# Optimization experiments

Measured on AMD Instinct MI355X. Metric: run time of the kernel, lower is better.

The kernel has to match this reference:

```python
import jax, jax.numpy as jnp
import numpy as np

B, S, T = 64, 49, 32
ENC, HID, EMB, VOCAB = 512, 512, 512, 32000
ATT = HID  # attention_dim = hidden_size in __init__


def setup_inputs() -> dict:
    key = jax.random.key(0)
    ks = jax.random.split(key, 20)
    def lin(k, out_d, in_d):
        s = 1.0 / np.sqrt(in_d)
        kw, kb = jax.random.split(k)
        return (jax.random.uniform(kw, (out_d, in_d), jnp.float32, -s, s),
                jax.random.uniform(kb, (out_d,), jnp.float32, -s, s))
    W_ih, b_ih = lin(ks[0], 3 * HID, EMB + ENC)
    W_hh, b_hh = lin(ks[1], 3 * HID, HID)
    W_out, b_out = lin(ks[2], VOCAB, HID)
    W_init, b_init = lin(ks[3], HID, ENC)
    W_beta, b_beta = lin(ks[4], ENC, HID)
    W_ea, b_ea = lin(ks[5], ATT, ENC)
    W_da, b_da = lin(ks[6], ATT, HID)
    W_fa, b_fa = lin(ks[7], 1, ATT)
    emb = jax.random.normal(ks[8], (VOCAB, EMB), jnp.float32)
    feats = jax.random.normal(ks[9], (B, S, ENC), jnp.float32)
    seq = jax.random.randint(ks[10], (B, T), 0, VOCAB)
    length = jax.random.randint(ks[11], (B,), 1, T + 1).at[0].set(T)
    return dict(feats=feats, seq=seq, length=length, emb=emb,
                W_ih=W_ih, b_ih=b_ih, W_hh=W_hh, b_hh=b_hh,
                W_out=W_out, b_out=b_out, W_init=W_init, b_init=b_init,
                W_beta=W_beta, b_beta=b_beta, W_ea=W_ea, b_ea=b_ea,
                W_da=W_da, b_da=b_da, W_fa=W_fa, b_fa=b_fa)


def _forward(feats, seq, length, emb, W_ih, b_ih, W_hh, b_hh, W_out, b_out,
             W_init, b_init, W_beta, b_beta, W_ea, b_ea, W_da, b_da, W_fa, b_fa):
    Tlen = seq.shape[1]
    embed_seq = emb[seq]                      # [B, T, EMB]
    embed_seq = jnp.swapaxes(embed_seq, 0, 1)  # [T, B, EMB]
    # active[t, b] = (length[b] > t); equivalent to torch's sorted shrinking batch
    active = (jnp.arange(Tlen)[:, None] < length[None, :])  # [T, B] bool
    h0 = jnp.mean(feats, axis=1) @ W_init.T + b_init         # [B, HID]
    scope0 = jnp.ones(feats.shape[:2], feats.dtype)          # [B, S]
    att1 = feats @ W_ea.T + b_ea                              # [B, S, ATT], hoisted

    def gru_cell(x, h):
        gi = x @ W_ih.T + b_ih
        gh = h @ W_hh.T + b_hh
        ir, iz, inn = jnp.split(gi, 3, axis=1)
        hr, hz, hn = jnp.split(gh, 3, axis=1)
        r = jax.nn.sigmoid(ir + hr)
        z = jax.nn.sigmoid(iz + hz)
        n = jnp.tanh(inn + r * hn)
        return (1.0 - z) * n + z * h

    def step(carry, xs):
        h, scope = carry
        embed_t, act = xs                     # [B, EMB], [B] bool
        actf = act[:, None].astype(h.dtype)
        att2 = h @ W_da.T + b_da              # [B, ATT]
        att = (jax.nn.relu(att1 + att2[:, None, :]) @ W_fa.T).squeeze(-1) + b_fa  # [B, S]
        alpha = jax.nn.softmax(att, axis=1)
        alpha_tilde = scope * alpha
        scope = jnp.where(act[:, None], scope * (1.0 - alpha), scope)
        awe = jnp.einsum('bse,bs->be', feats, alpha)          # [B, ENC]
        gate = jax.nn.sigmoid(h @ W_beta.T + b_beta)
        x = jnp.concatenate([embed_t, gate * awe], axis=1)
        h_new = gru_cell(x, h)
        h = jnp.where(act[:, None], h_new, h)
        preds = h_new @ W_out.T + b_out
        out_t = preds * actf
        alpha_out = alpha_tilde * actf
        return (h, scope), (out_t, alpha_out)

    (_, _), (output, alphas) = jax.lax.scan(step, (h0, scope0), (embed_seq, active))
    output = jnp.swapaxes(output, 0, 1)   # [B, T, VOCAB]
    alphas = jnp.swapaxes(alphas, 0, 1)   # [B, T, S]
    return output, alphas


def reference(feats, seq, length, emb, W_ih, b_ih, W_hh, b_hh, W_out, b_out,
              W_init, b_init, W_beta, b_beta, W_ea, b_ea, W_da, b_da, W_fa, b_fa):
    return _forward(feats, seq, length, emb, W_ih, b_ih, W_hh, b_hh, W_out, b_out,
                    W_init, b_init, W_beta, b_beta, W_ea, b_ea, W_da, b_da, W_fa, b_fa)
```

## Files before the change

### kernel.cpp

```cpp
#include <hip/hip_runtime.h>
#include <cstdint>
#include <cstddef>

#define B_   64
#define S_   49
#define T_   32
#define D_   512
#define V_   32000
#define G3   1536
#define NBLK 64

typedef float v4f   __attribute__((ext_vector_type(4)));
typedef int   i32x4 __attribute__((ext_vector_type(4)));
typedef _Float16 f16;
typedef _Float16 f16x8 __attribute__((ext_vector_type(8)));
typedef _Float16 f16x4 __attribute__((ext_vector_type(4)));

__device__ __forceinline__ float sigm(float x) { return 1.f / (1.f + __expf(-x)); }

__device__ __forceinline__ uint64_t ld_a64(const void* p) {
  return __hip_atomic_load((const uint64_t*)p, __ATOMIC_RELAXED, __HIP_MEMORY_SCOPE_AGENT);
}
__device__ __forceinline__ void st_a64(void* p, uint64_t v) {
  __hip_atomic_store((uint64_t*)p, v, __ATOMIC_RELAXED, __HIP_MEMORY_SCOPE_AGENT);
}
__device__ __forceinline__ uint32_t ld_a32(const void* p) {
  return __hip_atomic_load((const uint32_t*)p, __ATOMIC_RELAXED, __HIP_MEMORY_SCOPE_AGENT);
}
__device__ __forceinline__ void st_a32(void* p, uint32_t v) {
  __hip_atomic_store((uint32_t*)p, v, __ATOMIC_RELAXED, __HIP_MEMORY_SCOPE_AGENT);
}

__global__ __launch_bounds__(256) void k_cvt16(const float* __restrict__ in,
                                               f16* __restrict__ out) {
  int i = (blockIdx.x * 256 + threadIdx.x) * 8;
  float4 a = *(const float4*)(in + i);
  float4 b = *(const float4*)(in + i + 4);
  f16x8 o;
  o[0] = (f16)a.x; o[1] = (f16)a.y; o[2] = (f16)a.z; o[3] = (f16)a.w;
  o[4] = (f16)b.x; o[5] = (f16)b.y; o[6] = (f16)b.z; o[7] = (f16)b.w;
  *(f16x8*)(out + i) = o;
}

__global__ __launch_bounds__(128) void k_embed(const float* __restrict__ emb,
    const int* __restrict__ seq, const int* __restrict__ length,
    f16* __restrict__ xemb16, float* __restrict__ actmask) {
  int m = blockIdx.x;
  int t = m >> 6, b = m & 63;
  int idx = seq[b * T_ + t];
  float4 v = ((const float4*)(emb + (size_t)idx * D_))[threadIdx.x];
  f16x4 o;
  o[0] = (f16)v.x; o[1] = (f16)v.y; o[2] = (f16)v.z; o[3] = (f16)v.w;
  *(f16x4*)(xemb16 + (size_t)m * D_ + threadIdx.x * 4) = o;
  if (threadIdx.x == 0) actmask[b * T_ + t] = (t < length[b]) ? 1.f : 0.f;
}

__global__ __launch_bounds__(256) void k_hmean(const float* __restrict__ feats,
    float* __restrict__ hmean) {
  int b = blockIdx.x, tid = threadIdx.x;
  for (int e = tid; e < D_; e += 256) {
    float s = 0.f;
    for (int si = 0; si < S_; ++si) s += feats[((size_t)b * S_ + si) * D_ + e];
    hmean[b * D_ + e] = s * (1.f / 49.f);
  }
}

__global__ __launch_bounds__(256) void k_gemm_f32(
    float* __restrict__ C, const float* __restrict__ X, const float* __restrict__ W,
    const float* __restrict__ bias, int N, int K, int ldw) {
  __shared__ __align__(16) float XsT[32][68];
  __shared__ __align__(16) float WsT[32][68];
  const int nbase = blockIdx.x * 64, mbase = blockIdx.y * 64;
  const int tid = threadIdx.x;
  const int lr = tid >> 2;
  const int lk = (tid & 3) * 8;
  const int ty = tid >> 4, tx = tid & 15;
  float acc[4][4] = {};
  for (int k0 = 0; k0 < K; k0 += 32) {
    {
      const float* xs = X + (size_t)(mbase + lr) * K + k0 + lk;
      const float* wsrc = W + (size_t)(nbase + lr) * ldw + k0 + lk;
      float4 x0 = *(const float4*)xs, x1 = *(const float4*)(xs + 4);
      float4 w0 = *(const float4*)wsrc, w1 = *(const float4*)(wsrc + 4);
      XsT[lk + 0][lr] = x0.x; XsT[lk + 1][lr] = x0.y; XsT[lk + 2][lr] = x0.z; XsT[lk + 3][lr] = x0.w;
      XsT[lk + 4][lr] = x1.x; XsT[lk + 5][lr] = x1.y; XsT[lk + 6][lr] = x1.z; XsT[lk + 7][lr] = x1.w;
      WsT[lk + 0][lr] = w0.x; WsT[lk + 1][lr] = w0.y; WsT[lk + 2][lr] = w0.z; WsT[lk + 3][lr] = w0.w;
      WsT[lk + 4][lr] = w1.x; WsT[lk + 5][lr] = w1.y; WsT[lk + 6][lr] = w1.z; WsT[lk + 7][lr] = w1.w;
    }
    __syncthreads();
    #pragma unroll
    for (int kk = 0; kk < 32; ++kk) {
      float4 a4 = *(const float4*)&XsT[kk][ty * 4];
      float4 w4 = *(const float4*)&WsT[kk][tx * 4];
      float av[4] = {a4.x, a4.y, a4.z, a4.w};
      float wv[4] = {w4.x, w4.y, w4.z, w4.w};
      #pragma unroll
      for (int i = 0; i < 4; ++i)
        #pragma unroll
        for (int j = 0; j < 4; ++j)
          acc[i][j] = fmaf(av[i], wv[j], acc[i][j]);
    }
    __syncthreads();
  }
  #pragma unroll
  for (int i = 0; i < 4; ++i) {
    int m = mbase + ty * 4 + i;
    int n = nbase + tx * 4;
    float4 o;
    o.x = acc[i][0] + bias[n + 0];
    o.y = acc[i][1] + bias[n + 1];
    o.z = acc[i][2] + bias[n + 2];
    o.w = acc[i][3] + bias[n + 3];
    *(float4*)&C[(size_t)m * N + n] = o;
  }
}

__global__ __launch_bounds__(256) void k_gemm16b(
    const f16* __restrict__ A, const f16* __restrict__ Bw,
    const float* __restrict__ bias, float* __restrict__ out, int N) {
  __shared__ __align__(16) f16 As[128 * 32];
  __shared__ __align__(16) f16 Bs[128 * 32];
  const int nb = blockIdx.x * 128, mb = blockIdx.y * 128;
  const int tid = threadIdx.x;
  const int l = tid & 63, w = tid >> 6;
  const int wr = w >> 1, wc = w & 1;
  const int lm = l & 15;
  const int kc = l >> 4;
  const int rchunk = (kc ^ ((lm >> 1) & 3)) * 8;
  v4f acc[4][4];
  #pragma unroll
  for (int mi = 0; mi < 4; ++mi)
    #pragma unroll
    for (int ni = 0; ni < 4; ++ni)
      acc[mi][ni] = (v4f){0.f, 0.f, 0.f, 0.f};
  i32x4 ra[2], rb[2];
  auto LD = [&](int k0) {
    #pragma unroll
    for (int i = 0; i < 2; ++i) {
      int ch = i * 256 + tid;
      int row = ch >> 2, cq = ch & 3;
      ra[i] = *(const i32x4*)&A[(size_t)(mb + row) * 512 + k0 + cq * 8];
      rb[i] = *(const i32x4*)&Bw[(size_t)(nb + row) * 512 + k0 + cq * 8];
    }
  };
  LD(0);
  for (int k0 = 0; k0 < 512; k0 += 32) {
    #pragma unroll
    for (int i = 0; i < 2; ++i) {
      int ch = i * 256 + tid;
      int row = ch >> 2, cq = ch & 3;
      int sc = (cq ^ ((row >> 1) & 3)) * 8;
      *(i32x4*)&As[row * 32 + sc] = ra[i];
      *(i32x4*)&Bs[row * 32 + sc] = rb[i];
    }
    __syncthreads();
    if (k0 < 480) LD(k0 + 32);
    f16x8 af[4], bf[4];
    #pragma unroll
    for (int mi = 0; mi < 4; ++mi)
      af[mi] = *(const f16x8*)&As[(wr * 64 + mi * 16 + lm) * 32 + rchunk];
    #pragma unroll
    for (int ni = 0; ni < 4; ++ni)
      bf[ni] = *(const f16x8*)&Bs[(wc * 64 + ni * 16 + lm) * 32 + rchunk];
    #pragma unroll
    for (int mi = 0; mi < 4; ++mi)
      #pragma unroll
      for (int ni = 0; ni < 4; ++ni)
        acc[mi][ni] = __builtin_amdgcn_mfma_f32_16x16x32_f16(af[mi], bf[ni], acc[mi][ni], 0, 0, 0);
    __syncthreads();
  }
  #pragma unroll
  for (int ni = 0; ni < 4; ++ni) {
    int n = nb + wc * 64 + ni * 16 + lm;
    float bo = bias[n];
    #pragma unroll
    for (int mi = 0; mi < 4; ++mi) {
      int m0 = mb + wr * 64 + mi * 16 + (l >> 4) * 4;
      #pragma unroll
      for (int r = 0; r < 4; ++r)
        out[(size_t)(m0 + r) * N + n] = acc[mi][ni][r] + bo;
    }
  }
}

__global__ __launch_bounds__(256) void k_packW(
    const float* __restrict__ Wda, const float* __restrict__ Wbe,
    const float* __restrict__ Whh, const float* __restrict__ Wih,
    f16* __restrict__ Wp1, f16* __restrict__ Wp2, f16* __restrict__ Wp3) {
  int K = blockIdx.x, tid = threadIdx.x;
  for (int idx = tid; idx < 40 * 512; idx += 256) {
    int r = idx >> 9, e = idx & 511;
    float v;
    if (r < 8)       v = Wda[(size_t)(8 * K + r) * D_ + e];
    else if (r < 16) v = Wbe[(size_t)(8 * K + r - 8) * D_ + e];
    else if (r < 24) v = Whh[(size_t)(8 * K + r - 16) * D_ + e];
    else if (r < 32) v = Whh[(size_t)(512 + 8 * K + r - 24) * D_ + e];
    else             v = Whh[(size_t)(1024 + 8 * K + r - 32) * D_ + e];
    Wp1[(size_t)K * 20480 + idx] = (f16)v;
  }
  for (int idx = tid; idx < 24 * 512; idx += 256) {
    int r = idx >> 9, e = idx & 511;
    int g = r >> 3, jj = r & 7;
    float v = Wih[(size_t)(g * 512 + 8 * K + jj) * 1024 + 512 + e];
    Wp2[(size_t)K * 12288 + idx] = (f16)v;
  }
  for (int idx = tid; idx < 24 * 512; idx += 256) {
    int rl = idx >> 9, e = idx & 511;
    int r = K * 24 + rl;
    Wp3[(size_t)r * 512 + e] = (f16)Wih[(size_t)r * 1024 + e];
  }
}

__global__ __launch_bounds__(256) void k_packF(
    const float* __restrict__ feats, const float* __restrict__ att1,
    const float* __restrict__ h0,
    f16* __restrict__ feats16, f16* __restrict__ att116, f16* __restrict__ h16) {
  const int NF = B_ * S_ * D_;
  for (size_t i = blockIdx.x * 256 + threadIdx.x; i < 2 * NF + B_ * D_;
       i += (size_t)gridDim.x * 256) {
    if (i < NF)           feats16[i] = (f16)feats[i];
    else if (i < 2 * NF)  att116[i - NF] = (f16)att1[i - NF];
    else                  h16[i - 2 * NF] = (f16)h0[i - 2 * NF];
  }
}

__global__ __launch_bounds__(256) void k_packG(
    const float* __restrict__ gi_embed, float* __restrict__ gi_pack) {
  for (size_t i = blockIdx.x * 256 + threadIdx.x; i < (size_t)T_ * 64 * 32 * 64;
       i += (size_t)gridDim.x * 256) {
    int b = i & 63;
    int slot = (i >> 6) & 31;
    int Kb = (i >> 11) & 63;
    int t = i >> 17;
    if (slot < 24) {
      int g8 = slot >> 3, jj = slot & 7;
      gi_pack[i] = gi_embed[((size_t)t * 64 + b) * G3 + g8 * 512 + 8 * Kb + jj];
    }
  }
}

__device__ __forceinline__ void wait_flags64(const int* __restrict__ flags,
                                             int target, int tid) {
  if (tid < 64) {
    while (!__all((int)ld_a32(flags + tid * 16) >= target))
      __builtin_amdgcn_s_sleep(2);
  }
  __syncthreads();
}

__device__ __forceinline__ void set_flag(int* slot, int val, int tid) {
  __syncthreads();
  if (tid == 0) st_a32(slot, (uint32_t)val);
}

__device__ __forceinline__ void stage_fast(const f16* __restrict__ src,
                                           uint4* __restrict__ hs, int tid) {
  const i32x4* s = (const i32x4*)src;
  #pragma unroll
  for (int half = 0; half < 2; ++half) {
    i32x4 v[8];
    #pragma unroll
    for (int i = 0; i < 8; ++i) {
      int g = (half * 8 + i) * 256 + tid;
      asm volatile("global_load_dwordx4 %0, %1, off sc0 sc1"
                   : "=v"(v[i]) : "v"(s + g));
    }
    asm volatile("s_waitcnt vmcnt(0)" ::: "memory");
    __builtin_amdgcn_sched_barrier(0);
    #pragma unroll
    for (int i = 0; i < 8; ++i) {
      int g = (half * 8 + i) * 256 + tid;
      int b = g >> 6, c = g & 63;
      *(i32x4*)&hs[b * 64 + (c ^ (b & 7))] = v[i];
    }
  }
}

__global__ __launch_bounds__(256, 1) void k_recur(
    const f16* __restrict__ Wp1, const f16* __restrict__ Wp2,
    const f16* __restrict__ att116, const f16* __restrict__ feats16,
    const float* __restrict__ gi_pack,
    const float* __restrict__ b_da, const float* __restrict__ b_beta,
    const float* __restrict__ b_hh,
    const float* __restrict__ W_fa, const float* __restrict__ b_fa,
    const int* __restrict__ length,
    f16* __restrict__ h16, f16* __restrict__ xg16,
    float* __restrict__ att2g,
    float* __restrict__ alphas, f16* __restrict__ Hbuf,
    int* __restrict__ flags) {
  __shared__ __align__(16) uint4 lds_all[8704];
  __shared__ float gh_lds[24 * 72];
  __shared__ float gix_lds[24 * 72];
  __shared__ float att2_s[512];
  __shared__ float gate_s[512];
  __shared__ float att_s[64];
  __shared__ float alpha_s[64];
  uint4* hs = lds_all;
  uint4* W1 = lds_all + 4096;
  uint4* W2 = lds_all + 6656;
  float* attp = (float*)(lds_all + 8192);

  const int K = blockIdx.x, tid = threadIdx.x;
  const int w = tid >> 6, l = tid & 63;
  const int lm = l & 15, c4 = l >> 4;
  const int bq = tid & 63, jg = tid >> 6;
  const int jj0 = 2 * jg, jj1 = 2 * jg + 1;
  int* flagA = flags;
  int* flagB = flags + 1024;
  int* flagC = flags + 2048;

  {
    const uint4* s1 = (const uint4*)(Wp1 + (size_t)K * 20480);
    const uint4* s2 = (const uint4*)(Wp2 + (size_t)K * 12288);
    #pragma unroll
    for (int i = 0; i < 10; ++i) {
      int g = i * 256 + tid;
      int s = g >> 6, c = g & 63;
      W1[s * 64 + (c ^ (s & 7))] = s1[g];
    }
    #pragma unroll
    for (int i = 0; i < 6; ++i) {
      int g = i * 256 + tid;
      int s = g >> 6, c = g & 63;
      W2[s * 64 + (c ^ (s & 7))] = s2[g];
    }
  }
  const int lenB = length[K];
  const float bfa0 = b_fa[0];
  const int lb = length[bq];
  const float bhr0 = b_hh[8 * K + jj0],        bhr1 = b_hh[8 * K + jj1];
  const float bhz0 = b_hh[512 + 8 * K + jj0],  bhz1 = b_hh[512 + 8 * K + jj1];
  const float bhn0 = b_hh[1024 + 8 * K + jj0], bhn1 = b_hh[1024 + 8 * K + jj1];
  float scope_r = 1.f;
  __syncthreads();

  for (int t = 0; t < T_; ++t) {
    if (t) wait_flags64(flagC, t, tid);
    stage_fast(h16, hs, tid);
    __syncthreads();
    float hold0, hold1;
    {
      f16x8 hv = __builtin_bit_cast(f16x8, hs[bq * 64 + (K ^ (bq & 7))]);
      hold0 = (float)hv[jj0]; hold1 = (float)hv[jj1];
    }
    {
      v4f a0 = {0.f, 0.f, 0.f, 0.f};
      int bb = w * 16 + lm;
      #pragma unroll
      for (int kt = 0; kt < 16; ++kt) {
        int ca = kt * 4 + c4;
        f16x8 av = __builtin_bit_cast(f16x8, hs[bb * 64 + (ca ^ (bb & 7))]);
        f16x8 b0 = __builtin_bit_cast(f16x8, W1[lm * 64 + (ca ^ (lm & 7))]);
        a0 = __builtin_amdgcn_mfma_f32_16x16x32_f16(av, b0, a0, 0, 0, 0);
      }
      #pragma unroll
      for (int r = 0; r < 4; ++r)
        attp[(w * 16 + c4 * 4 + r) * 16 + lm] = a0[r];
    }
    __syncthreads();
    #pragma unroll
    for (int q = 0; q < 2; ++q) {
      int pp = tid * 2 + q;
      int bat = pp >> 3, pi = pp & 7;
      float2 f2;
      f2.x = attp[bat * 16 + 2 * pi];
      f2.y = attp[bat * 16 + 2 * pi + 1];
      size_t idx = (size_t)bat * 512 +
                   ((pi < 4) ? (4 * K + pi) : (256 + 4 * K + (pi - 4)));
      st_a64((uint64_t*)att2g + idx, __builtin_bit_cast(uint64_t, f2));
    }
    set_flag(flagA + K * 16, t + 1, tid);
    {
      v4f a1 = {0.f,0.f,0.f,0.f}, a2 = {0.f,0.f,0.f,0.f};
      int bb = w * 16 + lm;
      #pragma unroll
      for (int kt = 0; kt < 16; ++kt) {
        int ca = kt * 4 + c4;
        f16x8 av = __builtin_bit_cast(f16x8, hs[bb * 64 + (ca ^ (bb & 7))]);
        f16x8 b1 = __builtin_bit_cast(f16x8, W1[(16 + lm) * 64 + (ca ^ ((16 + lm) & 7))]);
        f16x8 b2 = __builtin_bit_cast(f16x8, W1[(32 + lm) * 64 + (ca ^ ((32 + lm) & 7))]);
        a1 = __builtin_amdgcn_mfma_f32_16x16x32_f16(av, b1, a1, 0, 0, 0);
        a2 = __builtin_amdgcn_mfma_f32_16x16x32_f16(av, b2, a2, 0, 0, 0);
      }
      #pragma unroll
      for (int r = 0; r < 4; ++r) {
        int bat = w * 16 + c4 * 4 + r;
        gh_lds[lm * 72 + bat] = a1[r];
        if (lm < 8) gh_lds[(16 + lm) * 72 + bat] = a2[r];
      }
    }
    wait_flags64(flagA, t + 1, tid);
    {
      bool act = t < lenB;
      const uint64_t* arow2 = (const uint64_t*)att2g + (size_t)K * 512;
      for (int c = tid; c < 512; c += 256) {
        float2 f = __builtin_bit_cast(float2, ld_a64(arow2 + c));
        int a0i = 2 * c;
        if (a0i < 512) {
          att2_s[a0i]     = f.x + b_da[a0i];
          att2_s[a0i + 1] = f.y + b_da[a0i + 1];
        } else {
          int gi = a0i - 512;
          gate_s[gi]     = sigm(f.x + b_beta[gi]);
          gate_s[gi + 1] = sigm(f.y + b_beta[gi + 1]);
        }
      }
      __syncthreads();
      for (int s = w; s < S_; s += 4) {
        const f16x8* arow = (const f16x8*)(att116 + ((size_t)K * S_ + s) * D_);
        int a0i = l * 8;
        f16x8 av = arow[l];
        float p = 0.f;
        #pragma unroll
        for (int jx = 0; jx < 8; ++jx) {
          float v = (float)av[jx] + att2_s[a0i + jx];
          v = v > 0.f ? v : 0.f;
          p = fmaf(v, W_fa[a0i + jx], p);
        }
        #pragma unroll
        for (int off = 32; off > 0; off >>= 1) p += __shfl_xor(p, off, 64);
        if (l == 0) att_s[s] = p + bfa0;
      }
      __syncthreads();
      if (tid < 64) {
        float x = (tid < S_) ? att_s[tid] : -1e30f;
        float m = x;
        #pragma unroll
        for (int off = 32; off > 0; off >>= 1) m = fmaxf(m, __shfl_xor(m, off, 64));
        float e = (tid < S_) ? __expf(x - m) : 0.f;
        float su = e;
        #pragma unroll
        for (int off = 32; off > 0; off >>= 1) su += __shfl_xor(su, off, 64);
        if (tid < S_) alpha_s[tid] = e / su;
      }
      __syncthreads();
      if (tid < S_) {
        float al = alpha_s[tid];
        alphas[((size_t)K * T_ + t) * S_ + tid] = act ? scope_r * al : 0.f;
        scope_r = act ? scope_r * (1.f - al) : scope_r;
      }
      if (tid < 128) {
        int e0 = tid * 4;
        float s0 = 0.f, s1 = 0.f, s2 = 0.f, s3 = 0.f;
        #pragma unroll 7
        for (int s = 0; s < S_; ++s) {
          float al = alpha_s[s];
          f16x4 fv = *(const f16x4*)(feats16 + ((size_t)K * S_ + s) * D_ + e0);
          s0 = fmaf(al, (float)fv[0], s0);
          s1 = fmaf(al, (float)fv[1], s1);
          s2 = fmaf(al, (float)fv[2], s2);
          s3 = fmaf(al, (float)fv[3], s3);
        }
        f16x4 o;
        o[0] = (f16)(gate_s[e0 + 0] * s0);
        o[1] = (f16)(gate_s[e0 + 1] * s1);
        o[2] = (f16)(gate_s[e0 + 2] * s2);
        o[3] = (f16)(gate_s[e0 + 3] * s3);
        st_a64((uint64_t*)xg16 + (size_t)K * 128 + tid,
               __builtin_bit_cast(uint64_t, o));
      }
    }
    set_flag(flagB + K * 16, t + 1, tid);
    wait_flags64(flagB, t + 1, tid);
    stage_fast(xg16, hs, tid);
    __syncthreads();
    {
      v4f c0 = {0.f,0.f,0.f,0.f}, c1 = {0.f,0.f,0.f,0.f};
      int bb = w * 16 + lm;
      #pragma unroll
      for (int kt = 0; kt < 16; ++kt) {
        int ca = kt * 4 + c4;
        f16x8 av = __builtin_bit_cast(f16x8, hs[bb * 64 + (ca ^ (bb & 7))]);
        f16x8 b0 = __builtin_bit_cast(f16x8, W2[lm * 64 + (ca ^ (lm & 7))]);
        f16x8 b1 = __builtin_bit_cast(f16x8, W2[(16 + lm) * 64 + (ca ^ ((16 + lm) & 7))]);
        c0 = __builtin_amdgcn_mfma_f32_16x16x32_f16(av, b0, c0, 0, 0, 0);
        c1 = __builtin_amdgcn_mfma_f32_16x16x32_f16(av, b1, c1, 0, 0, 0);
      }
      #pragma unroll
      for (int r = 0; r < 4; ++r) {
        int bat = w * 16 + c4 * 4 + r;
        gix_lds[lm * 72 + bat] = c0[r];
        if (lm < 8) gix_lds[(16 + lm) * 72 + bat] = c1[r];
      }
    }
    __syncthreads();
    {
      const float* gp = gi_pack + (size_t)(t * 64 + K) * 2048;
      float r0 = sigm(gix_lds[jj0 * 72 + bq] + gp[jj0 * 64 + bq] + gh_lds[jj0 * 72 + bq] + bhr0);
      float r1 = sigm(gix_lds[jj1 * 72 + bq] + gp[jj1 * 64 + bq] + gh_lds[jj1 * 72 + bq] + bhr1);
      float z0 = sigm(gix_lds[(8 + jj0) * 72 + bq] + gp[(8 + jj0) * 64 + bq] + gh_lds[(8 + jj0) * 72 + bq] + bhz0);
      float z1 = sigm(gix_lds[(8 + jj1) * 72 + bq] + gp[(8 + jj1) * 64 + bq] + gh_lds[(8 + jj1) * 72 + bq] + bhz1);
      float n0 = tanhf(gix_lds[(16 + jj0) * 72 + bq] + gp[(16 + jj0) * 64 + bq] + r0 * (gh_lds[(16 + jj0) * 72 + bq] + bhn0));
      float n1 = tanhf(gix_lds[(16 + jj1) * 72 + bq] + gp[(16 + jj1) * 64 + bq] + r1 * (gh_lds[(16 + jj1) * 72 + bq] + bhn1));
      float hn0 = (1.f - z0) * n0 + z0 * hold0;
      float hn1 = (1.f - z1) * n1 + z1 * hold1;
      bool act = t < lb;
      unsigned short u0 = __builtin_bit_cast(unsigned short, (f16)(act ? hn0 : hold0));
      unsigned short u1 = __builtin_bit_cast(unsigned short, (f16)(act ? hn1 : hold1));
      st_a32((uint32_t*)h16 + bq * 256 + 4 * K + jg,
             (uint32_t)u0 | ((uint32_t)u1 << 16));
      unsigned short p0 = __builtin_bit_cast(unsigned short, (f16)hn0);
      unsigned short p1 = __builtin_bit_cast(unsigned short, (f16)hn1);
      ((uint32_t*)Hbuf)[((size_t)bq * T_ + t) * 256 + 4 * K + jg] =
          (uint32_t)p0 | ((uint32_t)p1 << 16);
    }
    set_flag(flagC + K * 16, t + 1, tid);
  }
}

__global__ __launch_bounds__(256) void k_outgemm(
    const f16* __restrict__ Hb, const f16* __restrict__ Wb,
    const float* __restrict__ b_out, const float* __restrict__ actmask,
    float* __restrict__ out) {
  __shared__ __align__(16) f16 As[128 * 32];
  __shared__ __align__(16) f16 Bs[128 * 32];
  const int bid = blockIdx.x;
  const int swz = (bid & 7) * 500 + (bid >> 3);
  const int mb = (swz & 15) * 128;
  const int nb = (swz >> 4) * 128;
  const int tid = threadIdx.x;
  const int l = tid & 63, w = tid >> 6;
  const int wr = w >> 1, wc = w & 1;
  const int lm = l & 15;
  const int kc = l >> 4;
  const int rchunk = (kc ^ ((lm >> 1) & 3)) * 8;
  v4f acc[4][4];
  #pragma unroll
  for (int mi = 0; mi < 4; ++mi)
    #pragma unroll
    for (int ni = 0; ni < 4; ++ni)
      acc[mi][ni] = (v4f){0.f, 0.f, 0.f, 0.f};
  i32x4 ra[2], rb[2];
  auto LD = [&](int k0) {
    #pragma unroll
    for (int i = 0; i < 2; ++i) {
      int ch = i * 256 + tid;
      int row = ch >> 2, cq = ch & 3;
      ra[i] = *(const i32x4*)&Hb[(size_t)(mb + row) * 512 + k0 + cq * 8];
      rb[i] = *(const i32x4*)&Wb[(size_t)(nb + row) * 512 + k0 + cq * 8];
    }
  };
  LD(0);
  for (int k0 = 0; k0 < 512; k0 += 32) {
    #pragma unroll
    for (int i = 0; i < 2; ++i) {
      int ch = i * 256 + tid;
      int row = ch >> 2, cq = ch & 3;
      int sc = (cq ^ ((row >> 1) & 3)) * 8;
      *(i32x4*)&As[row * 32 + sc] = ra[i];
      *(i32x4*)&Bs[row * 32 + sc] = rb[i];
    }
    __syncthreads();
    if (k0 < 480) LD(k0 + 32);
    f16x8 af[4], bf[4];
    #pragma unroll
    for (int mi = 0; mi < 4; ++mi)
      af[mi] = *(const f16x8*)&As[(wr * 64 + mi * 16 + lm) * 32 + rchunk];
    #pragma unroll
    for (int ni = 0; ni < 4; ++ni)
      bf[ni] = *(const f16x8*)&Bs[(wc * 64 + ni * 16 + lm) * 32 + rchunk];
    #pragma unroll
    for (int mi = 0; mi < 4; ++mi)
      #pragma unroll
      for (int ni = 0; ni < 4; ++ni)
        acc[mi][ni] = __builtin_amdgcn_mfma_f32_16x16x32_f16(af[mi], bf[ni], acc[mi][ni], 0, 0, 0);
    __syncthreads();
  }
  #pragma unroll
  for (int ni = 0; ni < 4; ++ni) {
    int n = nb + wc * 64 + ni * 16 + lm;
    float bo = b_out[n];
    #pragma unroll
    for (int mi = 0; mi < 4; ++mi) {
      int m0 = mb + wr * 64 + mi * 16 + (l >> 4) * 4;
      #pragma unroll
      for (int r = 0; r < 4; ++r) {
        int m = m0 + r;
        out[(size_t)m * V_ + n] = actmask[m] * (acc[mi][ni][r] + bo);
      }
    }
  }
}

extern "C" void kernel_launch(void* const* d_in, const int* in_sizes, int n_in,
                              void* d_out, int out_size, void* d_ws, size_t ws_size,
                              hipStream_t stream) {
  const float* feats  = (const float*)d_in[0];
  const int*   seq    = (const int*)d_in[1];
  const int*   length = (const int*)d_in[2];
  const float* emb    = (const float*)d_in[3];
  const float* W_ih   = (const float*)d_in[4];
  const float* b_ih   = (const float*)d_in[5];
  const float* W_hh   = (const float*)d_in[6];
  const float* b_hh   = (const float*)d_in[7];
  const float* W_out  = (const float*)d_in[8];
  const float* b_out  = (const float*)d_in[9];
  const float* W_init = (const float*)d_in[10];
  const float* b_init = (const float*)d_in[11];
  const float* W_beta = (const float*)d_in[12];
  const float* b_beta = (const float*)d_in[13];
  const float* W_ea   = (const float*)d_in[14];
  const float* b_ea   = (const float*)d_in[15];
  const float* W_da   = (const float*)d_in[16];
  const float* b_da   = (const float*)d_in[17];
  const float* W_fa   = (const float*)d_in[18];
  const float* b_fa   = (const float*)d_in[19];

  float* out    = (float*)d_out;
  float* alphas = out + (size_t)B_ * T_ * V_;

  float* ws = (float*)d_ws;
  int*   flags    = (int*)ws;        ws += 4096;
  float* h0       = ws;              ws += B_ * D_;
  float* hmean    = ws;              ws += B_ * D_;
  float* actmask  = ws;              ws += B_ * T_;
  float* att2g    = ws;              ws += B_ * 1024;
  float* gi_embed = ws;              ws += (size_t)B_ * T_ * G3;
  float* gi_pack  = ws;              ws += (size_t)T_ * 64 * 32 * 64;
  float* att1     = ws;              ws += (size_t)B_ * S_ * D_;
  f16* fp = (f16*)ws;
  f16* Woutb   = fp;  fp += (size_t)V_ * D_;
  f16* Hbuf    = fp;  fp += (size_t)B_ * T_ * D_;
  f16* Wp1     = fp;  fp += (size_t)64 * 20480;
  f16* Wp2     = fp;  fp += (size_t)64 * 12288;
  f16* Wp3     = fp;  fp += (size_t)G3 * D_;
  f16* xemb16  = fp;  fp += (size_t)B_ * T_ * D_;
  f16* feats16 = fp;  fp += (size_t)B_ * S_ * D_;
  f16* att116  = fp;  fp += (size_t)B_ * S_ * D_;
  f16* h16     = fp;  fp += B_ * D_;
  f16* xg16    = fp;  fp += B_ * D_;

  hipMemsetAsync(flags, 0, 16384, stream);

  k_cvt16<<<(V_ * D_) / 2048, 256, 0, stream>>>(W_out, Woutb);
  k_embed<<<B_ * T_, 128, 0, stream>>>(emb, seq, length, xemb16, actmask);
  k_hmean<<<B_, 256, 0, stream>>>(feats, hmean);
  k_gemm_f32<<<dim3(8, 1), 256, 0, stream>>>(h0, hmean, W_init, b_init, 512, 512, 512);
  k_gemm_f32<<<dim3(8, 49), 256, 0, stream>>>(att1, feats, W_ea, b_ea, 512, 512, 512);
  k_packW<<<64, 256, 0, stream>>>(W_da, W_beta, W_hh, W_ih, Wp1, Wp2, Wp3);
  k_gemm16b<<<dim3(12, 16), 256, 0, stream>>>(xemb16, Wp3, b_ih, gi_embed, G3);
  k_packF<<<2048, 256, 0, stream>>>(feats, att1, h0, feats16, att116, h16);
  k_packG<<<2048, 256, 0, stream>>>(gi_embed, gi_pack);

  k_recur<<<NBLK, 256, 0, stream>>>(Wp1, Wp2, att116, feats16, gi_pack,
      b_da, b_beta, b_hh, W_fa, b_fa, length,
      h16, xg16, att2g, alphas, Hbuf, flags);

  k_outgemm<<<4000, 256, 0, stream>>>(Hbuf, Woutb, b_out, actmask, out);
}
```

Measured before the change: 1.008 ms.

## Fuse packing into GEMM epilogues, use fp16 MFMA for att1, restructure recurrence overlap

Replaces the fp32 att1 GEMM with an fp16 MFMA GEMM that writes att116 directly, and makes the gi_embed GEMM scatter straight into the packed gi_pack layout, removing the k_packG pass and the intermediate buffers. Inside the recurrent kernel it hoists W_fa and bias loads out of the time loop and prefetches att1 rows before the flag wait. It also moves the n-gate hidden MFMA to after the second flag set so it overlaps the wait, removes s_sleep from the spin loop, and issues all 16 staging loads at once. These changes trade extra register pressure and busier spinning for less serialized work per step and fewer preprocessing kernels; att1 now takes an fp16 path throughout.

```diff
diff --git a/kernel.cpp b/kernel.cpp
--- a/kernel.cpp
+++ b/kernel.cpp
@@ -115,60 +115,63 @@
   }
 }
 
-__global__ __launch_bounds__(256) void k_gemm16b(
+#define GEMM16_CORE                                                            \
+  __shared__ __align__(16) f16 As[128 * 32];                                   \
+  __shared__ __align__(16) f16 Bs[128 * 32];                                   \
+  const int tid = threadIdx.x;                                                 \
+  const int l = tid & 63, w = tid >> 6;                                        \
+  const int wr = w >> 1, wc = w & 1;                                           \
+  const int lm = l & 15;                                                       \
+  const int kc = l >> 4;                                                       \
+  const int rchunk = (kc ^ ((lm >> 1) & 3)) * 8;                               \
+  v4f acc[4][4];                                                               \
+  _Pragma("unroll")                                                            \
+  for (int mi = 0; mi < 4; ++mi)                                               \
+    _Pragma("unroll")                                                          \
+    for (int ni = 0; ni < 4; ++ni)                                             \
+      acc[mi][ni] = (v4f){0.f, 0.f, 0.f, 0.f};                                 \
+  i32x4 ra[2], rb[2];                                                          \
+  auto LD = [&](int k0) {                                                      \
+    _Pragma("unroll")                                                          \
+    for (int i = 0; i < 2; ++i) {                                              \
+      int ch = i * 256 + tid;                                                  \
+      int row = ch >> 2, cq = ch & 3;                                          \
+      ra[i] = *(const i32x4*)&A[(size_t)(mb + row) * 512 + k0 + cq * 8];       \
+      rb[i] = *(const i32x4*)&Bw[(size_t)(nb + row) * 512 + k0 + cq * 8];      \
+    }                                                                          \
+  };                                                                           \
+  LD(0);                                                                       \
+  for (int k0 = 0; k0 < 512; k0 += 32) {                                       \
+    _Pragma("unroll")                                                          \
+    for (int i = 0; i < 2; ++i) {                                              \
+      int ch = i * 256 + tid;                                                  \
+      int row = ch >> 2, cq = ch & 3;                                          \
+      int sc = (cq ^ ((row >> 1) & 3)) * 8;                                    \
+      *(i32x4*)&As[row * 32 + sc] = ra[i];                                     \
+      *(i32x4*)&Bs[row * 32 + sc] = rb[i];                                     \
+    }                                                                          \
+    __syncthreads();                                                           \
+    if (k0 < 480) LD(k0 + 32);                                                 \
+    f16x8 af[4], bf[4];                                                        \
+    _Pragma("unroll")                                                          \
+    for (int mi = 0; mi < 4; ++mi)                                             \
+      af[mi] = *(const f16x8*)&As[(wr * 64 + mi * 16 + lm) * 32 + rchunk];     \
+    _Pragma("unroll")                                                          \
+    for (int ni = 0; ni < 4; ++ni)                                             \
+      bf[ni] = *(const f16x8*)&Bs[(wc * 64 + ni * 16 + lm) * 32 + rchunk];     \
+    _Pragma("unroll")                                                          \
+    for (int mi = 0; mi < 4; ++mi)                                             \
+      _Pragma("unroll")                                                        \
+      for (int ni = 0; ni < 4; ++ni)                                           \
+        acc[mi][ni] = __builtin_amdgcn_mfma_f32_16x16x32_f16(af[mi], bf[ni], acc[mi][ni], 0, 0, 0); \
+    __syncthreads();                                                           \
+  }
+
+__global__ __launch_bounds__(256) void k_gemm16f(
     const f16* __restrict__ A, const f16* __restrict__ Bw,
-    const float* __restrict__ bias, float* __restrict__ out, int N) {
-  __shared__ __align__(16) f16 As[128 * 32];
-  __shared__ __align__(16) f16 Bs[128 * 32];
+    const float* __restrict__ bias, f16* __restrict__ out) {
   const int nb = blockIdx.x * 128, mb = blockIdx.y * 128;
-  const int tid = threadIdx.x;
-  const int l = tid & 63, w = tid >> 6;
-  const int wr = w >> 1, wc = w & 1;
-  const int lm = l & 15;
-  const int kc = l >> 4;
-  const int rchunk = (kc ^ ((lm >> 1) & 3)) * 8;
-  v4f acc[4][4];
-  #pragma unroll
-  for (int mi = 0; mi < 4; ++mi)
-    #pragma unroll
-    for (int ni = 0; ni < 4; ++ni)
-      acc[mi][ni] = (v4f){0.f, 0.f, 0.f, 0.f};
-  i32x4 ra[2], rb[2];
-  auto LD = [&](int k0) {
-    #pragma unroll
-    for (int i = 0; i < 2; ++i) {
-      int ch = i * 256 + tid;
-      int row = ch >> 2, cq = ch & 3;
-      ra[i] = *(const i32x4*)&A[(size_t)(mb + row) * 512 + k0 + cq * 8];
-      rb[i] = *(const i32x4*)&Bw[(size_t)(nb + row) * 512 + k0 + cq * 8];
-    }
-  };
-  LD(0);
-  for (int k0 = 0; k0 < 512; k0 += 32) {
-    #pragma unroll
-    for (int i = 0; i < 2; ++i) {
-      int ch = i * 256 + tid;
-      int row = ch >> 2, cq = ch & 3;
-      int sc = (cq ^ ((row >> 1) & 3)) * 8;
-      *(i32x4*)&As[row * 32 + sc] = ra[i];
-      *(i32x4*)&Bs[row * 32 + sc] = rb[i];
-    }
-    __syncthreads();
-    if (k0 < 480) LD(k0 + 32);
-    f16x8 af[4], bf[4];
-    #pragma unroll
-    for (int mi = 0; mi < 4; ++mi)
-      af[mi] = *(const f16x8*)&As[(wr * 64 + mi * 16 + lm) * 32 + rchunk];
-    #pragma unroll
-    for (int ni = 0; ni < 4; ++ni)
-      bf[ni] = *(const f16x8*)&Bs[(wc * 64 + ni * 16 + lm) * 32 + rchunk];
-    #pragma unroll
-    for (int mi = 0; mi < 4; ++mi)
-      #pragma unroll
-      for (int ni = 0; ni < 4; ++ni)
-        acc[mi][ni] = __builtin_amdgcn_mfma_f32_16x16x32_f16(af[mi], bf[ni], acc[mi][ni], 0, 0, 0);
-    __syncthreads();
-  }
+  GEMM16_CORE
   #pragma unroll
   for (int ni = 0; ni < 4; ++ni) {
     int n = nb + wc * 64 + ni * 16 + lm;
@@ -177,8 +180,33 @@
     for (int mi = 0; mi < 4; ++mi) {
       int m0 = mb + wr * 64 + mi * 16 + (l >> 4) * 4;
       #pragma unroll
+      for (int r = 0; r < 4; ++r) {
+        int m = m0 + r;
+        if (m < B_ * S_) out[(size_t)m * 512 + n] = (f16)(acc[mi][ni][r] + bo);
+      }
+    }
+  }
+}
+
+__global__ __launch_bounds__(256) void k_gemm16g(
+    const f16* __restrict__ A, const f16* __restrict__ Bw,
+    const float* __restrict__ bias, float* __restrict__ out) {
+  const int nb = blockIdx.x * 128, mb = blockIdx.y * 128;
+  GEMM16_CORE
+  #pragma unroll
+  for (int ni = 0; ni < 4; ++ni) {
+    int n = nb + wc * 64 + ni * 16 + lm;
+    float bo = bias[n];
+    int gate = n >> 9, rem = n & 511;
+    int Kb = rem >> 3, jl = rem & 7;
+    #pragma unroll
+    for (int mi = 0; mi < 4; ++mi) {
+      int m0 = mb + wr * 64 + mi * 16 + (l >> 4) * 4;
+      int t = m0 >> 6, b0q = m0 & 63;
+      float* dst = out + (((size_t)t * 64 + Kb) * 32 + gate * 8 + jl) * 64 + b0q;
+      #pragma unroll
       for (int r = 0; r < 4; ++r)
-        out[(size_t)(m0 + r) * N + n] = acc[mi][ni][r] + bo;
+        dst[r] = acc[mi][ni][r] + bo;
     }
   }
 }
@@ -212,38 +240,20 @@
 }
 
 __global__ __launch_bounds__(256) void k_packF(
-    const float* __restrict__ feats, const float* __restrict__ att1,
-    const float* __restrict__ h0,
-    f16* __restrict__ feats16, f16* __restrict__ att116, f16* __restrict__ h16) {
+    const float* __restrict__ feats, const float* __restrict__ h0,
+    f16* __restrict__ feats16, f16* __restrict__ h16) {
   const int NF = B_ * S_ * D_;
-  for (size_t i = blockIdx.x * 256 + threadIdx.x; i < 2 * NF + B_ * D_;
+  for (size_t i = blockIdx.x * 256 + threadIdx.x; i < NF + B_ * D_;
        i += (size_t)gridDim.x * 256) {
-    if (i < NF)           feats16[i] = (f16)feats[i];
-    else if (i < 2 * NF)  att116[i - NF] = (f16)att1[i - NF];
-    else                  h16[i - 2 * NF] = (f16)h0[i - 2 * NF];
-  }
-}
-
-__global__ __launch_bounds__(256) void k_packG(
-    const float* __restrict__ gi_embed, float* __restrict__ gi_pack) {
-  for (size_t i = blockIdx.x * 256 + threadIdx.x; i < (size_t)T_ * 64 * 32 * 64;
-       i += (size_t)gridDim.x * 256) {
-    int b = i & 63;
-    int slot = (i >> 6) & 31;
-    int Kb = (i >> 11) & 63;
-    int t = i >> 17;
-    if (slot < 24) {
-      int g8 = slot >> 3, jj = slot & 7;
-      gi_pack[i] = gi_embed[((size_t)t * 64 + b) * G3 + g8 * 512 + 8 * Kb + jj];
-    }
+    if (i < NF) feats16[i] = (f16)feats[i];
+    else        h16[i - NF] = (f16)h0[i - NF];
   }
 }
 
 __device__ __forceinline__ void wait_flags64(const int* __restrict__ flags,
                                              int target, int tid) {
   if (tid < 64) {
-    while (!__all((int)ld_a32(flags + tid * 16) >= target))
-      __builtin_amdgcn_s_sleep(2);
+    while (!__all((int)ld_a32(flags + tid * 16) >= target)) {}
   }
   __syncthreads();
 }
@@ -256,23 +266,19 @@
 __device__ __forceinline__ void stage_fast(const f16* __restrict__ src,
                                            uint4* __restrict__ hs, int tid) {
   const i32x4* s = (const i32x4*)src;
+  i32x4 v[16];
   #pragma unroll
-  for (int half = 0; half < 2; ++half) {
-    i32x4 v[8];
-    #pragma unroll
-    for (int i = 0; i < 8; ++i) {
-      int g = (half * 8 + i) * 256 + tid;
-      asm volatile("global_load_dwordx4 %0, %1, off sc0 sc1"
-                   : "=v"(v[i]) : "v"(s + g));
-    }
-    asm volatile("s_waitcnt vmcnt(0)" ::: "memory");
-    __builtin_amdgcn_sched_barrier(0);
-    #pragma unroll
-    for (int i = 0; i < 8; ++i) {
-      int g = (half * 8 + i) * 256 + tid;
-      int b = g >> 6, c = g & 63;
-      *(i32x4*)&hs[b * 64 + (c ^ (b & 7))] = v[i];
-    }
+  for (int i = 0; i < 16; ++i) {
+    asm volatile("global_load_dwordx4 %0, %1, off sc0 sc1"
+                 : "=v"(v[i]) : "v"(s + i * 256 + tid));
+  }
+  asm volatile("s_waitcnt vmcnt(0)" ::: "memory");
+  __builtin_amdgcn_sched_barrier(0);
+  #pragma unroll
+  for (int i = 0; i < 16; ++i) {
+    int g = i * 256 + tid;
+    int b = g >> 6, c = g & 63;
+    *(i32x4*)&hs[b * 64 + (c ^ (b & 7))] = v[i];
   }
 }
 
@@ -331,6 +337,14 @@
   const float bhr0 = b_hh[8 * K + jj0],        bhr1 = b_hh[8 * K + jj1];
   const float bhz0 = b_hh[512 + 8 * K + jj0],  bhz1 = b_hh[512 + 8 * K + jj1];
   const float bhn0 = b_hh[1024 + 8 * K + jj0], bhn1 = b_hh[1024 + 8 * K + jj1];
+  float wfa[8];
+  {
+    int a0i = l * 8;
+    #pragma unroll
+    for (int jx = 0; jx < 8; ++jx) wfa[jx] = W_fa[a0i + jx];
+  }
+  const float bda0 = b_da[2 * tid], bda1 = b_da[2 * tid + 1];
+  const float bbe0 = b_beta[2 * tid], bbe1 = b_beta[2 * tid + 1];
   float scope_r = 1.f;
   __syncthreads();
 
@@ -370,56 +384,57 @@
       st_a64((uint64_t*)att2g + idx, __builtin_bit_cast(uint64_t, f2));
     }
     set_flag(flagA + K * 16, t + 1, tid);
-    {
-      v4f a1 = {0.f,0.f,0.f,0.f}, a2 = {0.f,0.f,0.f,0.f};
+    i32x4 attv[13];
+    #pragma unroll
+    for (int i = 0; i < 13; ++i) {
+      int s = w + 4 * i;
+      if (s < S_)
+        attv[i] = *(const i32x4*)(att116 + ((size_t)K * S_ + s) * D_ + l * 8);
+    }
+    {
+      v4f a1 = {0.f, 0.f, 0.f, 0.f};
       int bb = w * 16 + lm;
       #pragma unroll
       for (int kt = 0; kt < 16; ++kt) {
         int ca = kt * 4 + c4;
         f16x8 av = __builtin_bit_cast(f16x8, hs[bb * 64 + (ca ^ (bb & 7))]);
         f16x8 b1 = __builtin_bit_cast(f16x8, W1[(16 + lm) * 64 + (ca ^ ((16 + lm) & 7))]);
-        f16x8 b2 = __builtin_bit_cast(f16x8, W1[(32 + lm) * 64 + (ca ^ ((32 + lm) & 7))]);
         a1 = __builtin_amdgcn_mfma_f32_16x16x32_f16(av, b1, a1, 0, 0, 0);
-        a2 = __builtin_amdgcn_mfma_f32_16x16x32_f16(av, b2, a2, 0, 0, 0);
-      }
-      #pragma unroll
-      for (int r = 0; r < 4; ++r) {
-        int bat = w * 16 + c4 * 4 + r;
-        gh_lds[lm * 72 + bat] = a1[r];
-        if (lm < 8) gh_lds[(16 + lm) * 72 + bat] = a2[r];
-      }
+      }
+      #pragma unroll
+      for (int r = 0; r < 4; ++r)
+        gh_lds[lm * 72 + (w * 16 + c4 * 4 + r)] = a1[r];
     }
     wait_flags64(flagA, t + 1, tid);
     {
       bool act = t < lenB;
       const uint64_t* arow2 = (const uint64_t*)att2g + (size_t)K * 512;
-      for (int c = tid; c < 512; c += 256) {
-        float2 f = __builtin_bit_cast(float2, ld_a64(arow2 + c));
-        int a0i = 2 * c;
-        if (a0i < 512) {
-          att2_s[a0i]     = f.x + b_da[a0i];
-          att2_s[a0i + 1] = f.y + b_da[a0i + 1];
-        } else {
-          int gi = a0i - 512;
-          gate_s[gi]     = sigm(f.x + b_beta[gi]);
-          gate_s[gi + 1] = sigm(f.y + b_beta[gi + 1]);
+      {
+        float2 f = __builtin_bit_cast(float2, ld_a64(arow2 + tid));
+        att2_s[2 * tid]     = f.x + bda0;
+        att2_s[2 * tid + 1] = f.y + bda1;
+        float2 g = __builtin_bit_cast(float2, ld_a64(arow2 + tid + 256));
+        gate_s[2 * tid]     = sigm(g.x + bbe0);
+        gate_s[2 * tid + 1] = sigm(g.y + bbe1);
+      }
+      __syncthreads();
+      int a0i = l * 8;
+      #pragma unroll
+      for (int i = 0; i < 13; ++i) {
+        int s = w + 4 * i;
+        if (s < S_) {
+          f16x8 av = __builtin_bit_cast(f16x8, attv[i]);
+          float p = 0.f;
+          #pragma unroll
+          for (int jx = 0; jx < 8; ++jx) {
+            float v = (float)av[jx] + att2_s[a0i + jx];
+            v = v > 0.f ? v : 0.f;
+            p = fmaf(v, wfa[jx], p);
+          }
+          #pragma unroll
+          for (int off = 32; off > 0; off >>= 1) p += __shfl_xor(p, off, 64);
+          if (l == 0) att_s[s] = p + bfa0;
         }
-      }
-      __syncthreads();
-      for (int s = w; s < S_; s += 4) {
-        const f16x8* arow = (const f16x8*)(att116 + ((size_t)K * S_ + s) * D_);
-        int a0i = l * 8;
-        f16x8 av = arow[l];
-        float p = 0.f;
-        #pragma unroll
-        for (int jx = 0; jx < 8; ++jx) {
-          float v = (float)av[jx] + att2_s[a0i + jx];
-          v = v > 0.f ? v : 0.f;
-          p = fmaf(v, W_fa[a0i + jx], p);
-        }
-        #pragma unroll
-        for (int off = 32; off > 0; off >>= 1) p += __shfl_xor(p, off, 64);
-        if (l == 0) att_s[s] = p + bfa0;
       }
       __syncthreads();
       if (tid < 64) {
@@ -461,6 +476,20 @@
       }
     }
     set_flag(flagB + K * 16, t + 1, tid);
+    {
+      v4f a2 = {0.f, 0.f, 0.f, 0.f};
+      int bb = w * 16 + lm;
+      #pragma unroll
+      for (int kt = 0; kt < 16; ++kt) {
+        int ca = kt * 4 + c4;
+        f16x8 av = __builtin_bit_cast(f16x8, hs[bb * 64 + (ca ^ (bb & 7))]);
+        f16x8 b2 = __builtin_bit_cast(f16x8, W1[(32 + lm) * 64 + (ca ^ ((32 + lm) & 7))]);
+        a2 = __builtin_amdgcn_mfma_f32_16x16x32_f16(av, b2, a2, 0, 0, 0);
+      }
+      #pragma unroll
+      for (int r = 0; r < 4; ++r)
+        if (lm < 8) gh_lds[(16 + lm) * 72 + (w * 16 + c4 * 4 + r)] = a2[r];
+    }
     wait_flags64(flagB, t + 1, tid);
     stage_fast(xg16, hs, tid);
     __syncthreads();
@@ -509,63 +538,14 @@
 }
 
 __global__ __launch_bounds__(256) void k_outgemm(
-    const f16* __restrict__ Hb, const f16* __restrict__ Wb,
+    const f16* __restrict__ A, const f16* __restrict__ Bw,
     const float* __restrict__ b_out, const float* __restrict__ actmask,
     float* __restrict__ out) {
-  __shared__ __align__(16) f16 As[128 * 32];
-  __shared__ __align__(16) f16 Bs[128 * 32];
   const int bid = blockIdx.x;
   const int swz = (bid & 7) * 500 + (bid >> 3);
   const int mb = (swz & 15) * 128;
   const int nb = (swz >> 4) * 128;
-  const int tid = threadIdx.x;
-  const int l = tid & 63, w = tid >> 6;
-  const int wr = w >> 1, wc = w & 1;
-  const int lm = l & 15;
-  const int kc = l >> 4;
-  const int rchunk = (kc ^ ((lm >> 1) & 3)) * 8;
-  v4f acc[4][4];
-  #pragma unroll
-  for (int mi = 0; mi < 4; ++mi)
-    #pragma unroll
-    for (int ni = 0; ni < 4; ++ni)
-      acc[mi][ni] = (v4f){0.f, 0.f, 0.f, 0.f};
-  i32x4 ra[2], rb[2];
-  auto LD = [&](int k0) {
-    #pragma unroll
-    for (int i = 0; i < 2; ++i) {
-      int ch = i * 256 + tid;
-      int row = ch >> 2, cq = ch & 3;
-      ra[i] = *(const i32x4*)&Hb[(size_t)(mb + row) * 512 + k0 + cq * 8];
-      rb[i] = *(const i32x4*)&Wb[(size_t)(nb + row) * 512 + k0 + cq * 8];
-    }
-  };
-  LD(0);
-  for (int k0 = 0; k0 < 512; k0 += 32) {
-    #pragma unroll
-    for (int i = 0; i < 2; ++i) {
-      int ch = i * 256 + tid;
-      int row = ch >> 2, cq = ch & 3;
-      int sc = (cq ^ ((row >> 1) & 3)) * 8;
-      *(i32x4*)&As[row * 32 + sc] = ra[i];
-      *(i32x4*)&Bs[row * 32 + sc] = rb[i];
-    }
-    __syncthreads();
-    if (k0 < 480) LD(k0 + 32);
-    f16x8 af[4], bf[4];
-    #pragma unroll
-    for (int mi = 0; mi < 4; ++mi)
-      af[mi] = *(const f16x8*)&As[(wr * 64 + mi * 16 + lm) * 32 + rchunk];
-    #pragma unroll
-    for (int ni = 0; ni < 4; ++ni)
-      bf[ni] = *(const f16x8*)&Bs[(wc * 64 + ni * 16 + lm) * 32 + rchunk];
-    #pragma unroll
-    for (int mi = 0; mi < 4; ++mi)
-      #pragma unroll
-      for (int ni = 0; ni < 4; ++ni)
-        acc[mi][ni] = __builtin_amdgcn_mfma_f32_16x16x32_f16(af[mi], bf[ni], acc[mi][ni], 0, 0, 0);
-    __syncthreads();
-  }
+  GEMM16_CORE
   #pragma unroll
   for (int ni = 0; ni < 4; ++ni) {
     int n = nb + wc * 64 + ni * 16 + lm;
@@ -615,17 +595,16 @@
   float* hmean    = ws;              ws += B_ * D_;
   float* actmask  = ws;              ws += B_ * T_;
   float* att2g    = ws;              ws += B_ * 1024;
-  float* gi_embed = ws;              ws += (size_t)B_ * T_ * G3;
   float* gi_pack  = ws;              ws += (size_t)T_ * 64 * 32 * 64;
-  float* att1     = ws;              ws += (size_t)B_ * S_ * D_;
   f16* fp = (f16*)ws;
   f16* Woutb   = fp;  fp += (size_t)V_ * D_;
   f16* Hbuf    = fp;  fp += (size_t)B_ * T_ * D_;
   f16* Wp1     = fp;  fp += (size_t)64 * 20480;
   f16* Wp2     = fp;  fp += (size_t)64 * 12288;
   f16* Wp3     = fp;  fp += (size_t)G3 * D_;
+  f16* Wea16   = fp;  fp += (size_t)D_ * D_;
   f16* xemb16  = fp;  fp += (size_t)B_ * T_ * D_;
-  f16* feats16 = fp;  fp += (size_t)B_ * S_ * D_;
+  f16* feats16 = fp;  fp += (size_t)3200 * D_;
   f16* att116  = fp;  fp += (size_t)B_ * S_ * D_;
   f16* h16     = fp;  fp += B_ * D_;
   f16* xg16    = fp;  fp += B_ * D_;
@@ -633,14 +612,14 @@
   hipMemsetAsync(flags, 0, 16384, stream);
 
   k_cvt16<<<(V_ * D_) / 2048, 256, 0, stream>>>(W_out, Woutb);
+  k_cvt16<<<(D_ * D_) / 2048, 256, 0, stream>>>(W_ea, Wea16);
   k_embed<<<B_ * T_, 128, 0, stream>>>(emb, seq, length, xemb16, actmask);
   k_hmean<<<B_, 256, 0, stream>>>(feats, hmean);
   k_gemm_f32<<<dim3(8, 1), 256, 0, stream>>>(h0, hmean, W_init, b_init, 512, 512, 512);
-  k_gemm_f32<<<dim3(8, 49), 256, 0, stream>>>(att1, feats, W_ea, b_ea, 512, 512, 512);
+  k_packF<<<2048, 256, 0, stream>>>(feats, h0, feats16, h16);
+  k_gemm16f<<<dim3(4, 25), 256, 0, stream>>>(feats16, Wea16, b_ea, att116);
   k_packW<<<64, 256, 0, stream>>>(W_da, W_beta, W_hh, W_ih, Wp1, Wp2, Wp3);
-  k_gemm16b<<<dim3(12, 16), 256, 0, stream>>>(xemb16, Wp3, b_ih, gi_embed, G3);
-  k_packF<<<2048, 256, 0, stream>>>(feats, att1, h0, feats16, att116, h16);
-  k_packG<<<2048, 256, 0, stream>>>(gi_embed, gi_pack);
+  k_gemm16g<<<dim3(12, 16), 256, 0, stream>>>(xemb16, Wp3, b_ih, gi_pack);
 
   k_recur<<<NBLK, 256, 0, stream>>>(Wp1, Wp2, att116, feats16, gi_pack,
       b_da, b_beta, b_hh, W_fa, b_fa, length,
```

New measurement: 922.9 us. 8.4% less time.
